# Performance work log

Hardware: AMD Instinct MI355X
Metric: run time of the kernel (lower is better)

The kernel has to match this reference:

```python
import jax, jax.numpy as jnp
import numpy as np

B, N, IN_DIM, OUT_DIM = 16, 2048, 512, 512

def _xavier(key, shape):
    bound = float(np.sqrt(6.0 / (shape[0] + shape[1])))
    return jax.random.uniform(key, shape, jnp.float32, -bound, bound)

def setup_inputs() -> dict:
    key = jax.random.key(0)
    kx, kk, kq, kv = jax.random.split(key, 4)
    return {
        "x": jax.random.normal(kx, (B, N, IN_DIM), jnp.float32),
        "W_key": _xavier(kk, (IN_DIM, OUT_DIM)),
        "W_query": _xavier(kq, (IN_DIM, OUT_DIM)),
        "W_value": _xavier(kv, (IN_DIM, OUT_DIM)),
    }

def reference(x, W_key, W_query, W_value):
    # projections: [B, N, out_dim]
    k = jnp.matmul(x, W_key)
    q = jnp.matmul(x, W_query)
    v = jnp.matmul(x, W_value)
    scale = jnp.sqrt(jnp.asarray(IN_DIM, jnp.float32))
    scores = jnp.einsum("bnd,bmd->bnm", q, k) / scale  # [B, N, N]
    weights = jax.nn.softmax(scores, axis=2)
    attn = jnp.einsum("bnm,bmd->bnd", weights, v)  # [B, N, out_dim]
    return jnp.mean(attn, axis=1)  # [B, out_dim]
```

## Files before the change

kernel.cpp:

```cpp
#include <hip/hip_runtime.h>
#include <hip/hip_bf16.h>
#include <hip/hip_fp16.h>
#include <stdint.h>

#define NB 16
#define NN 2048
#define ND 512
#define SSCALE 0.044194173824159216f

typedef unsigned short u16;
typedef unsigned int u32;
typedef float f32x4 __attribute__((ext_vector_type(4)));
typedef __bf16 bf16x8 __attribute__((ext_vector_type(8)));
typedef unsigned short u16x8 __attribute__((ext_vector_type(8)));

__device__ __forceinline__ float bf2f(u16 h) {
  union { u32 u; float f; } v; v.u = ((u32)h) << 16; return v.f;
}
__device__ __forceinline__ u16 f2bf(float f) {
  union { float f; u32 u; } v; v.f = f;
  u32 r = v.u + 0x7fffu + ((v.u >> 16) & 1u);
  return (u16)(r >> 16);
}
__device__ __forceinline__ u16 f2h(float f) {
  __half h = __float2half(f);
  union { __half h; u16 u; } v; v.h = h; return v.u;
}

__device__ __forceinline__ void async16(const void* g, void* l) {
  __builtin_amdgcn_global_load_lds(
      (const __attribute__((address_space(1))) u32*)g,
      (__attribute__((address_space(3))) u32*)l,
      16, 0, 0);
}

template <int MODE, bool AF32>
__global__ __launch_bounds__(256, 2) void gemm_bt(
    const void* __restrict__ Av, const u16* __restrict__ B, u16* __restrict__ C,
    float* __restrict__ Lrow, int lda, int ldb, int ldc, int K,
    long long sA, long long sB, long long sC, float cscale) {
  const int tid  = threadIdx.x;
  const int w    = tid >> 6;
  const int lane = tid & 63;
  const int wm   = w >> 1, wn = w & 1;
  const int lrow = lane & 15, quad = lane >> 4;
  const long long z = blockIdx.z;

  const float* Abf = (const float*)Av + z * sA + (size_t)blockIdx.y * 128 * lda;
  const u16*   Abh = (const u16*)Av   + z * sA + (size_t)blockIdx.y * 128 * lda;
  const u16*   Bb  = B + z * sB + (size_t)blockIdx.x * 128 * ldb;

  __shared__ __align__(16) u16 lds_a[128 * 32];
  __shared__ __align__(16) u16 lds_b[128 * 32];

  f32x4 acc[4][4];
#pragma unroll
  for (int i = 0; i < 4; i++)
#pragma unroll
    for (int j = 0; j < 4; j++) acc[i][j] = (f32x4){0.f, 0.f, 0.f, 0.f};

  for (int k0 = 0; k0 < K; k0 += 32) {
    if (k0) __syncthreads();
    if (AF32) {
      u16x8 va[2];
#pragma unroll
      for (int t = 0; t < 2; t++) {
        int ch  = t * 256 + tid;
        int row = ch >> 2;
        int cc  = (ch & 3) * 8;
        const float4* p = (const float4*)(Abf + (size_t)row * lda + k0 + cc);
        float4 f0 = p[0], f1 = p[1];
        u16x8 r;
        r[0] = f2bf(f0.x); r[1] = f2bf(f0.y); r[2] = f2bf(f0.z); r[3] = f2bf(f0.w);
        r[4] = f2bf(f1.x); r[5] = f2bf(f1.y); r[6] = f2bf(f1.z); r[7] = f2bf(f1.w);
        va[t] = r;
        async16(Bb + (size_t)row * ldb + k0 + cc, &lds_b[ch * 8]);
      }
#pragma unroll
      for (int t = 0; t < 2; t++) *(u16x8*)&lds_a[(t * 256 + tid) * 8] = va[t];
    } else {
#pragma unroll
      for (int t = 0; t < 2; t++) {
        int ch  = t * 256 + tid;
        int row = ch >> 2;
        int cc  = (ch & 3) * 8;
        async16(Abh + (size_t)row * lda + k0 + cc, &lds_a[ch * 8]);
        async16(Bb  + (size_t)row * ldb + k0 + cc, &lds_b[ch * 8]);
      }
    }
    __syncthreads();

    bf16x8 af[4], bfr[4];
#pragma unroll
    for (int i = 0; i < 4; i++) {
      af[i]  = *(const bf16x8*)&lds_a[(wm * 64 + i * 16 + lrow) * 32 + quad * 8];
      bfr[i] = *(const bf16x8*)&lds_b[(wn * 64 + i * 16 + lrow) * 32 + quad * 8];
    }
#pragma unroll
    for (int i = 0; i < 4; i++)
#pragma unroll
      for (int j = 0; j < 4; j++)
        acc[i][j] =
            __builtin_amdgcn_mfma_f32_16x16x32_bf16(af[i], bfr[j], acc[i][j], 0, 0, 0);
  }

  u16* Cb = C + z * sC + (size_t)blockIdx.y * 128 * ldc + (size_t)blockIdx.x * 128;
  if (MODE == 0) {
#pragma unroll
    for (int i = 0; i < 4; i++)
#pragma unroll
      for (int j = 0; j < 4; j++)
#pragma unroll
        for (int r = 0; r < 4; r++) {
          int row = wm * 64 + i * 16 + quad * 4 + r;
          int col = wn * 64 + j * 16 + lrow;
          Cb[(size_t)row * ldc + col] = f2bf(acc[i][j][r] * cscale);
        }
  } else {
    float* Lb = Lrow + z * NN + (size_t)blockIdx.y * 128;
#pragma unroll
    for (int i = 0; i < 4; i++)
#pragma unroll
      for (int r = 0; r < 4; r++) {
        int row = wm * 64 + i * 16 + quad * 4 + r;
        float rs = 0.f;
#pragma unroll
        for (int j = 0; j < 4; j++) {
          int col = wn * 64 + j * 16 + lrow;
          float e = __expf(fminf(acc[i][j][r] * cscale, 10.f));
          Cb[(size_t)row * ldc + col] = f2h(e);
          rs += e;
        }
        rs += __shfl_xor(rs, 1); rs += __shfl_xor(rs, 2);
        rs += __shfl_xor(rs, 4); rs += __shfl_xor(rs, 8);
        if (lrow == 0) atomicAdd(&Lb[row], rs);
      }
  }
}

__device__ __forceinline__ void stage_half(const u16* __restrict__ g, int ld,
                                           int row0, int k0,
                                           u16* __restrict__ l, int tid) {
  int r  = tid >> 3;
  int Lc = (tid & 7) ^ (r & 7);
  async16(g + (size_t)(row0 + r) * ld + k0 + Lc * 8, l + tid * 8);
  async16(g + (size_t)(row0 + 64 + r) * ld + k0 + Lc * 8, l + 4096 + tid * 8);
}

__device__ __forceinline__ bf16x8 ldf(const u16* __restrict__ h, int rbase,
                                      int lrow, int quad, int ks) {
  int rr = rbase + lrow;
  int pc = (ks * 4 + quad) ^ (lrow & 7);
  return *(const bf16x8*)&h[rr * 64 + pc * 8];
}

#define BAR() __builtin_amdgcn_s_barrier()
#define WAIT_LGKM()                                          \
  do {                                                       \
    asm volatile("s_waitcnt lgkmcnt(0)" ::: "memory");       \
    __builtin_amdgcn_sched_barrier(0);                       \
  } while (0)

#define READ_A(p, mh)                                                        \
  _Pragma("unroll") for (int i2 = 0; i2 < 4; ++i2)                           \
  _Pragma("unroll") for (int ks = 0; ks < 2; ++ks)                           \
      af[i2][ks] = ldf(sm + (p) * 32768 + wm * 8192, ((mh)*4 + i2) * 16,     \
                       lrow, quad, ks);

#define READ_B(p, nh)                                                        \
  _Pragma("unroll") for (int j2 = 0; j2 < 2; ++j2)                           \
  _Pragma("unroll") for (int ks = 0; ks < 2; ++ks)                           \
      bq[(nh)*2 + j2][ks] =                                                  \
          ldf(sm + (p) * 32768 + 16384 + (wn >> 1) * 8192,                   \
              (wn & 1) * 64 + ((nh)*2 + j2) * 16, lrow, quad, ks);

#define MFMA_Q(mh, nh)                                                       \
  __builtin_amdgcn_s_setprio(1);                                             \
  _Pragma("unroll") for (int i2 = 0; i2 < 4; ++i2)                           \
  _Pragma("unroll") for (int j2 = 0; j2 < 2; ++j2)                           \
  _Pragma("unroll") for (int ks = 0; ks < 2; ++ks)                           \
      acc[(mh)*4 + i2][(nh)*2 + j2] = __builtin_amdgcn_mfma_f32_16x16x32_bf16( \
          af[i2][ks], bq[(nh)*2 + j2][ks], acc[(mh)*4 + i2][(nh)*2 + j2],    \
          0, 0, 0);                                                          \
  __builtin_amdgcn_s_setprio(0);

#define STAGE_A(p, h, kt) \
  stage_half(Ab, lda, (h)*128, (kt)*64, sm + (p)*32768 + (h)*8192, tid)
#define STAGE_B(p, h, kt) \
  stage_half(Bb, ldb, (h)*128, (kt)*64, sm + (p)*32768 + 16384 + (h)*8192, tid)

template <int MODE>
__global__ __launch_bounds__(512, 2) void gemm256(
    const u16* __restrict__ A, const u16* __restrict__ B, u16* __restrict__ C,
    float* __restrict__ Lrow, int lda, int ldb, int ldc, int K,
    long long sA, long long sB, long long sC, float cscale) {
  const int tid  = threadIdx.x;
  const int wid  = tid >> 6, lane = tid & 63;
  const int wm   = wid >> 2, wn = wid & 3;
  const int lrow = lane & 15, quad = lane >> 4;
  const long long z = blockIdx.z;

  const u16* Ab = A + z * sA + (size_t)blockIdx.y * 256 * lda;
  const u16* Bb = B + z * sB + (size_t)blockIdx.x * 256 * ldb;

  __shared__ __align__(16) u16 sm[65536];

  f32x4 acc[8][4];
#pragma unroll
  for (int i = 0; i < 8; i++)
#pragma unroll
    for (int j = 0; j < 4; j++) acc[i][j] = (f32x4){0.f, 0.f, 0.f, 0.f};

  bf16x8 af[4][2];
  bf16x8 bq[4][2];

  const int NITER = K >> 7;

  STAGE_A(0, 0, 0); STAGE_A(0, 1, 0);
  STAGE_B(0, 0, 0); STAGE_B(0, 1, 0);
  STAGE_B(1, 0, 1); STAGE_B(1, 1, 1);
  asm volatile("s_waitcnt vmcnt(4)" ::: "memory");
  __builtin_amdgcn_sched_barrier(0);
  BAR();

  for (int it = 0; it < NITER; ++it) {
    const int t = 2 * it;
    const bool more = (it + 1 < NITER);

    READ_A(0, 0); READ_B(0, 0);
    STAGE_A(1, 0, t + 1);
    BAR(); WAIT_LGKM();
    MFMA_Q(0, 0);
    BAR();
    READ_B(0, 1);
    STAGE_A(1, 1, t + 1);
    BAR(); WAIT_LGKM();
    MFMA_Q(0, 1);
    BAR();
    READ_A(0, 1);
    if (more) STAGE_B(0, 0, t + 2);
    BAR(); WAIT_LGKM();
    MFMA_Q(1, 0);
    BAR();
    if (more) STAGE_B(0, 1, t + 2);
    BAR();
    MFMA_Q(1, 1);
    if (more) { asm volatile("s_waitcnt vmcnt(4)" ::: "memory"); }
    else      { asm volatile("s_waitcnt vmcnt(0)" ::: "memory"); }
    __builtin_amdgcn_sched_barrier(0);
    BAR();
    READ_A(1, 0); READ_B(1, 0);
    if (more) STAGE_A(0, 0, t + 2);
    BAR(); WAIT_LGKM();
    MFMA_Q(0, 0);
    BAR();
    READ_B(1, 1);
    if (more) STAGE_A(0, 1, t + 2);
    BAR(); WAIT_LGKM();
    MFMA_Q(0, 1);
    BAR();
    READ_A(1, 1);
    if (more) STAGE_B(1, 0, t + 3);
    BAR(); WAIT_LGKM();
    MFMA_Q(1, 0);
    BAR();
    if (more) STAGE_B(1, 1, t + 3);
    BAR();
    MFMA_Q(1, 1);
    if (more) {
      asm volatile("s_waitcnt vmcnt(4)" ::: "memory");
      __builtin_amdgcn_sched_barrier(0);
    }
    BAR();
  }

  u16* Cb = C + z * sC +
            (size_t)(blockIdx.y * 256 + wm * 128) * ldc +
            (size_t)blockIdx.x * 256 + wn * 64;
  if (MODE == 0) {
#pragma unroll
    for (int i = 0; i < 8; i++)
#pragma unroll
      for (int j = 0; j < 4; j++)
#pragma unroll
        for (int r = 0; r < 4; r++) {
          int row = i * 16 + quad * 4 + r;
          int col = j * 16 + lrow;
          Cb[(size_t)row * ldc + col] = f2bf(acc[i][j][r] * cscale);
        }
  } else {
    float* Lb = Lrow + z * NN + (size_t)blockIdx.y * 256 + wm * 128;
#pragma unroll
    for (int i = 0; i < 8; i++)
#pragma unroll
      for (int r = 0; r < 4; r++) {
        int row = i * 16 + quad * 4 + r;
        float rs = 0.f;
#pragma unroll
        for (int j = 0; j < 4; j++) {
          int col = j * 16 + lrow;
          float e = __expf(fminf(acc[i][j][r] * cscale, 10.f));
          Cb[(size_t)row * ldc + col] = f2h(e);
          rs += e;
        }
        rs += __shfl_xor(rs, 1); rs += __shfl_xor(rs, 2);
        rs += __shfl_xor(rs, 4); rs += __shfl_xor(rs, 8);
        if (lrow == 0) atomicAdd(&Lb[row], rs);
      }
  }
}

__global__ void cast_f32_bf16(const float* __restrict__ x, u16* __restrict__ xb) {
  size_t i = ((size_t)blockIdx.x * 256 + threadIdx.x) * 8;
  float4 f0 = *(const float4*)(x + i);
  float4 f1 = *(const float4*)(x + i + 4);
  u16x8 r;
  r[0] = f2bf(f0.x); r[1] = f2bf(f0.y); r[2] = f2bf(f0.z); r[3] = f2bf(f0.w);
  r[4] = f2bf(f1.x); r[5] = f2bf(f1.y); r[6] = f2bf(f1.z); r[7] = f2bf(f1.w);
  *(u16x8*)(xb + i) = r;
}

__global__ void col_sum(const __half* __restrict__ E, const float* __restrict__ L,
                        float* __restrict__ c) {
  int m2 = blockIdx.x * 256 + threadIdx.x;
  int n0 = blockIdx.y * 128;
  int z  = blockIdx.z;
  const __half2* Ep = (const __half2*)(E + ((size_t)z * NN + n0) * NN) + m2;
  const float* lp = L + (size_t)z * NN + n0;
  float a0 = 0.f, a1 = 0.f;
#pragma unroll 4
  for (int n = 0; n < 128; n++) {
    __half2 h = Ep[(size_t)n * (NN / 2)];
    float il = 1.0f / lp[n];
    a0 += __low2float(h) * il;
    a1 += __high2float(h) * il;
  }
  atomicAdd(&c[(size_t)z * NN + m2 * 2], a0);
  atomicAdd(&c[(size_t)z * NN + m2 * 2 + 1], a1);
}

__global__ void tx_accum(const u16* __restrict__ xb, const float* __restrict__ c,
                         float* __restrict__ t) {
  int b = blockIdx.x, mc = blockIdx.y, d = threadIdx.x;
  const u16* vp = xb + ((size_t)b * NN + mc * 128) * ND;
  const float* cp = c + b * NN + mc * 128;
  float a0 = 0.f, a1 = 0.f;
#pragma unroll 4
  for (int m = 0; m < 128; m++) {
    float cm = cp[m];
    a0 += cm * bf2f(vp[(size_t)m * ND + d]);
    a1 += cm * bf2f(vp[(size_t)m * ND + 256 + d]);
  }
  atomicAdd(&t[b * ND + d], a0);
  atomicAdd(&t[b * ND + 256 + d], a1);
}

__global__ void final_wv(const float* __restrict__ t, const float* __restrict__ Wv,
                         float* __restrict__ out) {
  int b = blockIdx.x, d = blockIdx.y * 256 + threadIdx.x;
  const float* tb = t + b * ND;
  float a = 0.f;
#pragma unroll 4
  for (int l = 0; l < ND; l++) a += tb[l] * Wv[(size_t)l * ND + d];
  out[b * ND + d] = a * (1.f / (float)NN);
}

extern "C" void kernel_launch(void* const* d_in, const int* in_sizes, int n_in,
                              void* d_out, int out_size, void* d_ws, size_t ws_size,
                              hipStream_t stream) {
  const float* x  = (const float*)d_in[0];
  const float* Wk = (const float*)d_in[1];
  const float* Wq = (const float*)d_in[2];
  const float* Wv = (const float*)d_in[3];
  float* out = (float*)d_out;

  char* ws = (char*)d_ws;
  size_t off = 0;
  float* L   = (float*)(ws + off); off += (size_t)NB * NN * 4;
  float* c   = (float*)(ws + off); off += (size_t)NB * NN * 4;
  float* t   = (float*)(ws + off); off += (size_t)NB * ND * 4;
  u16* Wqb   = (u16*)(ws + off);   off += (size_t)ND * ND * 2;
  u16* Mt    = (u16*)(ws + off);   off += (size_t)ND * ND * 2;
  const size_t small_total = off;

  const size_t XBSZ = (size_t)NB * NN * ND * 2;
  const size_t SB1  = (size_t)NN * NN * 2;
  u16* xb   = (u16*)(ws + small_total);
  u16* y    = (u16*)(ws + small_total + XBSZ);
  __half* E = (__half*)(ws + small_total + 2 * XBSZ);
  size_t srem = ws_size > small_total + 2 * XBSZ
              ? ws_size - small_total - 2 * XBSZ : 0;
  int chb = 0, sr = 128;
  if      (srem >= 16 * SB1) chb = 16;
  else if (srem >=  8 * SB1) chb = 8;
  else if (srem >=  4 * SB1) chb = 4;
  else if (srem >=  2 * SB1) chb = 2;
  else if (srem >=  1 * SB1) chb = 1;
  else {
    if      (srem >= (size_t)1024 * NN * 2) sr = 1024;
    else if (srem >= (size_t)512  * NN * 2) sr = 512;
    else if (srem >= (size_t)256  * NN * 2) sr = 256;
  }

  hipMemsetAsync(L, 0, (size_t)(2 * NB * NN + NB * ND) * sizeof(float), stream);

  cast_f32_bf16<<<8192, 256, 0, stream>>>(x, xb);
  cast_f32_bf16<<<128, 256, 0, stream>>>(Wq, Wqb);

  gemm_bt<0, true><<<dim3(4, 4, 1), 256, 0, stream>>>(
      Wk, Wqb, Mt, nullptr, ND, ND, ND, ND, 0, 0, 0, SSCALE);

  gemm256<0><<<dim3(2, 128, 1), 512, 0, stream>>>(
      xb, Mt, y, nullptr, ND, ND, ND, ND, 0, 0, 0, 1.0f);

  const long long sR = (long long)NN * ND;
  const long long sS = (long long)NN * NN;

  if (chb >= 1) {
    for (int cc = 0; cc < NB / chb; ++cc) {
      size_t o = (size_t)cc * chb * NN;
      gemm256<1><<<dim3(8, 8, chb), 512, 0, stream>>>(
          y + o * ND, xb + o * ND, (u16*)E, L + o, ND, ND, NN, ND,
          sR, sR, sS, 1.0f);
      col_sum<<<dim3(4, 16, chb), 256, 0, stream>>>(E, L + o, c + o);
    }
  } else if (sr >= 256) {
    for (int b = 0; b < NB; ++b) {
      for (int ch = 0; ch < NN / sr; ++ch) {
        size_t o = (size_t)b * NN + (size_t)ch * sr;
        gemm256<1><<<dim3(8, sr / 256, 1), 512, 0, stream>>>(
            y + o * ND, xb + (size_t)b * NN * ND, (u16*)E, L + o,
            ND, ND, NN, ND, 0, 0, 0, 1.0f);
        col_sum<<<dim3(4, sr / 128, 1), 256, 0, stream>>>(E, L + o, c + b * NN);
      }
    }
  } else {
    for (int b = 0; b < NB; ++b) {
      for (int ch = 0; ch < NN / sr; ++ch) {
        size_t o = (size_t)b * NN + (size_t)ch * sr;
        gemm_bt<1, false><<<dim3(16, sr / 128, 1), 256, 0, stream>>>(
            y + o * ND, xb + (size_t)b * NN * ND, (u16*)E, L + o,
            ND, ND, NN, ND, 0, 0, 0, 1.0f);
        col_sum<<<dim3(4, sr / 128, 1), 256, 0, stream>>>(E, L + o, c + b * NN);
      }
    }
  }

  tx_accum<<<dim3(NB, 16), 256, 0, stream>>>(xb, c, t);
  final_wv<<<dim3(NB, 2), 256, 0, stream>>>(t, Wv, out);
  (void)in_sizes; (void)n_in; (void)out_size;
}
```

Baseline: 348.8 us.

## Stage GEMM epilogue through swizzled LDS for coalesced stores; remap workgroups across XCDs

The 256x256 output tile is written into shared memory with an XOR swizzle, then copied to global memory with 16-byte coalesced vector stores instead of scattered 2-byte stores. The workgroup index is also remapped so consecutive tiles are grouped per chiplet (XCD round-robin), which is meant to improve L2 reuse of A/B panels. The cost is an extra barrier and an LDS round trip in the epilogue. The LDS buffer is reused after the main loop.

New measurement: 369.8 us. +6.0%, slower.

```diff
diff --git a/kernel.cpp b/kernel.cpp
--- a/kernel.cpp
+++ b/kernel.cpp
@@ -198,10 +198,18 @@
   const int wid  = tid >> 6, lane = tid & 63;
   const int wm   = wid >> 2, wn = wid & 3;
   const int lrow = lane & 15, quad = lane >> 4;
-  const long long z = blockIdx.z;
-
-  const u16* Ab = A + z * sA + (size_t)blockIdx.y * 256 * lda;
-  const u16* Bb = B + z * sB + (size_t)blockIdx.x * 256 * ldb;
+
+  const int ngx = gridDim.x, ngy = gridDim.y;
+  int h   = blockIdx.x + ngx * (blockIdx.y + ngy * blockIdx.z);
+  int nwg = ngx * ngy * (int)gridDim.z;
+  int l   = (nwg & 7) ? h : ((h & 7) * (nwg >> 3) + (h >> 3));
+  const int bxx = l % ngx;
+  const int t2q = l / ngx;
+  const int byy = t2q % ngy;
+  const long long z = t2q / ngy;
+
+  const u16* Ab = A + z * sA + (size_t)byy * 256 * lda;
+  const u16* Bb = B + z * sB + (size_t)bxx * 256 * ldb;
 
   __shared__ __align__(16) u16 sm[65536];
 
@@ -274,9 +282,7 @@
     BAR();
   }
 
-  u16* Cb = C + z * sC +
-            (size_t)(blockIdx.y * 256 + wm * 128) * ldc +
-            (size_t)blockIdx.x * 256 + wn * 64;
+  u16* Cb = C + z * sC + (size_t)byy * 256 * ldc + (size_t)bxx * 256;
   if (MODE == 0) {
 #pragma unroll
     for (int i = 0; i < 8; i++)
@@ -284,29 +290,43 @@
       for (int j = 0; j < 4; j++)
 #pragma unroll
         for (int r = 0; r < 4; r++) {
-          int row = i * 16 + quad * 4 + r;
-          int col = j * 16 + lrow;
-          Cb[(size_t)row * ldc + col] = f2bf(acc[i][j][r] * cscale);
+          int gr  = wm * 128 + i * 16 + quad * 4 + r;
+          int gc  = wn * 64 + j * 16 + lrow;
+          int c16 = gc >> 3;
+          int ph  = (c16 & ~7) | ((c16 ^ (gr >> 2)) & 7);
+          sm[gr * 256 + ph * 8 + (gc & 7)] = f2bf(acc[i][j][r] * cscale);
         }
   } else {
-    float* Lb = Lrow + z * NN + (size_t)blockIdx.y * 256 + wm * 128;
+    float* Lb = Lrow + z * NN + (size_t)byy * 256 + wm * 128;
 #pragma unroll
     for (int i = 0; i < 8; i++)
 #pragma unroll
       for (int r = 0; r < 4; r++) {
-        int row = i * 16 + quad * 4 + r;
+        int gr = wm * 128 + i * 16 + quad * 4 + r;
         float rs = 0.f;
 #pragma unroll
         for (int j = 0; j < 4; j++) {
-          int col = j * 16 + lrow;
+          int gc  = wn * 64 + j * 16 + lrow;
           float e = __expf(fminf(acc[i][j][r] * cscale, 10.f));
-          Cb[(size_t)row * ldc + col] = f2h(e);
+          int c16 = gc >> 3;
+          int ph  = (c16 & ~7) | ((c16 ^ (gr >> 2)) & 7);
+          sm[gr * 256 + ph * 8 + (gc & 7)] = f2h(e);
           rs += e;
         }
         rs += __shfl_xor(rs, 1); rs += __shfl_xor(rs, 2);
         rs += __shfl_xor(rs, 4); rs += __shfl_xor(rs, 8);
-        if (lrow == 0) atomicAdd(&Lb[row], rs);
-      }
+        if (lrow == 0) atomicAdd(&Lb[i * 16 + quad * 4 + r], rs);
+      }
+  }
+  __syncthreads();
+#pragma unroll
+  for (int k = 0; k < 16; ++k) {
+    int cch = tid + 512 * k;
+    int gr  = cch >> 5;
+    int c16 = cch & 31;
+    int ph  = (c16 & ~7) | ((c16 ^ (gr >> 2)) & 7);
+    f32x4 v = *(const f32x4*)&sm[gr * 256 + ph * 8];
+    *(f32x4*)&Cb[(size_t)gr * ldc + c16 * 8] = v;
   }
 }
 
```
